# Optimization experiments

Hardware: AMD Instinct MI355X
Metric: run time of the kernel (lower is better)

The kernel has to match this reference:

```python
import jax, jax.numpy as jnp
import numpy as np

TEMP = 0.1
THR = 0.01
W_F = 8
HW0_I = (640, 640)
HW0_F = (320, 320)
HW1_F = (320, 320)
HW0_C = (80, 80)
HW1_C = (80, 80)


def setup_inputs() -> dict:
    key = jax.random.key(0)
    ks = jax.random.split(key, 12)
    M, WW, C, N = 8192, W_F * W_F, 96, 2
    Hf, Wf = HW0_F
    Hc, Wc = HW0_C
    inp = {}
    inp['feat_f0_unfold'] = jax.random.normal(ks[0], (M, WW, C), jnp.float32)
    inp['feat_f1_unfold'] = jax.random.normal(ks[1], (M, WW, C), jnp.float32)
    inp['feat_f0_whole'] = jax.random.normal(ks[2], (N, C, Hf, Wf), jnp.float32)
    inp['feat_f1_whole'] = jax.random.normal(ks[3], (N, C, Hf, Wf), jnp.float32)
    inp['b_ids_c'] = jax.random.randint(ks[4], (M,), 0, N, jnp.int32)
    # interior coarse cells so 3x3 subpixel gathers never go out of bounds
    r0 = jax.random.randint(ks[5], (M,), 1, Hc - 1, jnp.int32)
    c0 = jax.random.randint(ks[6], (M,), 1, Wc - 1, jnp.int32)
    r1 = jax.random.randint(ks[7], (M,), 1, Hc - 1, jnp.int32)
    c1 = jax.random.randint(ks[8], (M,), 1, Wc - 1, jnp.int32)
    inp['i_ids_c'] = r0 * Wc + c0
    inp['j_ids_c'] = r1 * Wc + c1
    dim2 = 2 * 96
    inp['w1'] = jax.random.normal(ks[9], (dim2, dim2, 3, 3), jnp.float32) * 0.02
    inp['w2'] = jax.random.normal(ks[10], (dim2, dim2, 3, 3), jnp.float32) * 0.02
    inp['w3'] = jax.random.normal(ks[11], (4, dim2, 1, 1), jnp.float32) * 0.02
    return inp


def _conv(x, w, stride, pad):
    return jax.lax.conv_general_dilated(
        x, w, window_strides=(stride, stride), padding=pad,
        dimension_numbers=('NCHW', 'OIHW', 'NCHW'))


def _gather_patch(whole, b, y, x):
    # whole: [N, C, H, W]; returns 3x3 patches centered at (y, x) with zero pad,
    # matching F.unfold(kernel_size=3, stride=1, padding=1) + index_select.
    pad = jnp.pad(whole, ((0, 0), (0, 0), (1, 1), (1, 1)))
    off = jnp.arange(3, dtype=y.dtype)
    rows = y[:, None] + off  # padded row indices y-1..y+1 -> y..y+2
    cols = x[:, None] + off
    p = pad[b[:, None, None], :, rows[:, :, None], cols[:, None, :]]  # [M,3,3,C]
    return p.transpose(0, 3, 1, 2)  # [M, C, 3, 3]


def reference(feat_f0_unfold, feat_f1_unfold, feat_f0_whole, feat_f1_whole,
              b_ids_c, i_ids_c, j_ids_c, w1, w2, w3):
    M, WW, C = feat_f0_unfold.shape
    inv = C ** -0.5
    sim = jnp.einsum('mlc,msc->mls', feat_f0_unfold * inv, feat_f1_unfold * inv) / TEMP
    conf = jax.nn.softmax(sim, axis=1) * jax.nn.softmax(sim, axis=2)  # [M, WW, WW]

    # top-1 per fine conf matrix (threshold AND global argmax per matrix)
    flat = conf.reshape(M, WW * WW)
    idx = jnp.argmax(flat, axis=1)
    mconf = jnp.max(flat, axis=1)
    valid = mconf > THR
    i_ids = idx // WW
    j_ids = idx % WW

    scale_f_c = HW0_F[0] // HW0_C[0]
    mk0c = jnp.stack([i_ids_c % HW0_C[1], i_ids_c // HW0_C[1]], axis=1) * scale_f_c
    mk1c = jnp.stack([j_ids_c % HW1_C[1], j_ids_c // HW1_C[1]], axis=1) * scale_f_c
    win0 = jnp.stack([i_ids % W_F, i_ids // W_F], axis=1)
    win1 = jnp.stack([j_ids % W_F, j_ids // W_F], axis=1)
    mk0_uns = mk0c + win0 - W_F // 2  # [M, 2] (x, y) fine-res int coords
    mk1_uns = mk1c + win1 - W_F // 2

    f0 = _gather_patch(feat_f0_whole, b_ids_c, mk0_uns[:, 1], mk0_uns[:, 0])
    f1 = _gather_patch(feat_f1_whole, b_ids_c, mk1_uns[:, 1], mk1_uns[:, 0])
    x = jnp.concatenate([f0, f1], axis=1)  # [M, 192*2? -> 192] actually 2*96=192
    x = jax.nn.leaky_relu(_conv(x, w1, 1, [(1, 1), (1, 1)]))
    x = jax.nn.leaky_relu(_conv(x, w2, 3, 'VALID'))
    x = _conv(x, w3, 1, 'VALID').reshape(M, 4)
    sub0 = jnp.tanh(x[:, :2]) * 0.5
    sub1 = jnp.tanh(x[:, 2:]) * 0.5

    scale = HW0_I[0] / HW0_F[0]
    mkpts0_f = (mk0_uns.astype(sub0.dtype) + sub0) * scale
    mkpts1_f = (mk1_uns.astype(sub1.dtype) + sub1) * scale
    mconf = jnp.where(valid, mconf, 0.0)
    return conf, mconf, mkpts0_f, mkpts1_f, valid
```

## Files before the change

kernel.cpp:

```cpp
#include <hip/hip_runtime.h>
#include <hip/hip_bf16.h>
#include <math.h>

typedef __attribute__((ext_vector_type(4))) float f32x4;
typedef __attribute__((ext_vector_type(8))) short bf16x8;

#define M_TOT   8192
#define OFF_MCONF 33554432LL
#define OFF_MK0   33562624LL
#define OFF_MK1   33579008LL
#define OFF_VALID 33595392LL
#define SIM_SCALE 0.10416666666666667f

__device__ __forceinline__ short f2bf(float v) {
    __hip_bfloat16 h = __float2bfloat16(v);
    return *reinterpret_cast<short*>(&h);
}

__global__ void wprep(const float* __restrict__ w1, const float* __restrict__ w2,
                      short* __restrict__ o1, short* __restrict__ o2) {
    int i = blockIdx.x * 256 + threadIdx.x;
    if (i >= 2 * 331776) return;
    const float* src = (i < 331776) ? w1 : w2;
    short* dst       = (i < 331776) ? o1 : o2;
    int o = (i < 331776) ? i : i - 331776;
    int oc = o / 1728, r = o % 1728;
    int q = r / 192, ic = r % 192;
    dst[o] = f2bf(src[oc * 1728 + ic * 9 + q]);
}

__global__ __launch_bounds__(256) void stageA(const float* __restrict__ f0u,
                                              const float* __restrict__ f1u,
                                              const int* __restrict__ i_ids_c,
                                              const int* __restrict__ j_ids_c,
                                              float* __restrict__ out,
                                              int* __restrict__ mkws) {
    __shared__ float f0L[64 * 100];
    __shared__ float f1L[64 * 100];
    __shared__ float Rpart[16 * 64];
    __shared__ float Cpart[16 * 64];
    __shared__ float invR[64], invC[64];
    __shared__ float rv[256];
    __shared__ int   ri[256];

    const int m = blockIdx.x;
    const int t = threadIdx.x;
    const int lg = t >> 4, sg = t & 15;

    const float* g0 = f0u + (size_t)m * 6144;
    const float* g1 = f1u + (size_t)m * 6144;
    for (int v = t; v < 1536; v += 256) {
        int l = v / 24, c4 = (v % 24) * 4;
        *(f32x4*)&f0L[l * 100 + c4] = *(const f32x4*)(g0 + v * 4);
        *(f32x4*)&f1L[l * 100 + c4] = *(const f32x4*)(g1 + v * 4);
    }
    __syncthreads();

    float acc[4][4] = {};
#pragma unroll 2
    for (int k = 0; k < 96; k += 4) {
        f32x4 a[4], b[4];
#pragma unroll
        for (int i = 0; i < 4; ++i) a[i] = *(const f32x4*)&f0L[(lg + 16 * i) * 100 + k];
#pragma unroll
        for (int j = 0; j < 4; ++j) b[j] = *(const f32x4*)&f1L[(sg + 16 * j) * 100 + k];
#pragma unroll
        for (int i = 0; i < 4; ++i)
#pragma unroll
            for (int j = 0; j < 4; ++j) {
                acc[i][j] += a[i].x * b[j].x;
                acc[i][j] += a[i].y * b[j].y;
                acc[i][j] += a[i].z * b[j].z;
                acc[i][j] += a[i].w * b[j].w;
            }
    }

    float e[4][4];
    float rp[4] = {0.f, 0.f, 0.f, 0.f}, cp[4] = {0.f, 0.f, 0.f, 0.f};
#pragma unroll
    for (int i = 0; i < 4; ++i)
#pragma unroll
        for (int j = 0; j < 4; ++j) {
            float v = __expf(acc[i][j] * SIM_SCALE);
            e[i][j] = v;
            rp[i] += v;
            cp[j] += v;
        }
#pragma unroll
    for (int i = 0; i < 4; ++i) Rpart[sg * 64 + lg + 16 * i] = rp[i];
#pragma unroll
    for (int j = 0; j < 4; ++j) Cpart[lg * 64 + sg + 16 * j] = cp[j];
    __syncthreads();
    if (t < 64) {
        float sR = 0.f, sC = 0.f;
#pragma unroll
        for (int g = 0; g < 16; ++g) { sR += Rpart[g * 64 + t]; sC += Cpart[g * 64 + t]; }
        invR[t] = 1.0f / sR;
        invC[t] = 1.0f / sC;
    }
    __syncthreads();

    float bestv = -1.0f;
    int besti = 0;
    float* cbase = out + (size_t)m * 4096;
#pragma unroll
    for (int i = 0; i < 4; ++i) {
        int l = lg + 16 * i;
        float iR = invR[l];
#pragma unroll
        for (int j = 0; j < 4; ++j) {
            int s = sg + 16 * j;
            float c = (e[i][j] * iR) * (e[i][j] * invC[s]);
            cbase[l * 64 + s] = c;
            int fi = l * 64 + s;
            if (c > bestv || (c == bestv && fi < besti)) { bestv = c; besti = fi; }
        }
    }
    rv[t] = bestv; ri[t] = besti;
    __syncthreads();
    if (t < 64) {
#pragma unroll
        for (int g = 1; g < 4; ++g) {
            float v = rv[t + 64 * g]; int idx = ri[t + 64 * g];
            if (v > rv[t] || (v == rv[t] && idx < ri[t])) { rv[t] = v; ri[t] = idx; }
        }
    }
    __syncthreads();
    if (t == 0) {
        float bv = rv[0]; int bi = ri[0];
        for (int g = 1; g < 64; ++g) {
            float v = rv[g]; int idx = ri[g];
            if (v > bv || (v == bv && idx < bi)) { bv = v; bi = idx; }
        }
        bool valid = bv > 0.01f;
        out[OFF_MCONF + m] = valid ? bv : 0.0f;
        out[OFF_VALID + m] = valid ? 1.0f : 0.0f;
        int il = bi >> 6, js = bi & 63;
        int ic0 = i_ids_c[m], jc0 = j_ids_c[m];
        mkws[m * 4 + 0] = (ic0 % 80) * 4 + (il & 7) - 4;
        mkws[m * 4 + 1] = (ic0 / 80) * 4 + (il >> 3) - 4;
        mkws[m * 4 + 2] = (jc0 % 80) * 4 + (js & 7) - 4;
        mkws[m * 4 + 3] = (jc0 / 80) * 4 + (js >> 3) - 4;
    }
}

__global__ __launch_bounds__(256, 2) void stageB(const float* __restrict__ w0whole,
                                                 const float* __restrict__ w1whole,
                                                 const int* __restrict__ bids,
                                                 const int* __restrict__ mkws,
                                                 const short* __restrict__ w1b,
                                                 const short* __restrict__ w2b,
                                                 const float* __restrict__ w3,
                                                 float* __restrict__ out) {
    __shared__ short bufA[32000];
    __shared__ float bufC[16 * 196];
    __shared__ float xout[64];

    const int t = threadIdx.x;
    const int m0 = blockIdx.x * 16;
    const int lane = t & 63, wv = t >> 6;
    const int l16 = lane & 15, quad = lane >> 4;
    const int colb = wv * 48;

    for (int v = t; v < 16 * 200; v += 256) {
        int mm = v / 200, c = v % 200;
        bufA[mm * 2000 + 1800 + c] = 0;
    }
    for (int seg = t; seg < 9216; seg += 256) {
        int c = seg % 96;
        int r = seg / 96;
        int dy = r % 3;
        int mi = r / 3;
        int img = mi & 1;
        int m_loc = mi >> 1;
        int mg = m0 + m_loc;
        int b = bids[mg];
        int mkx = mkws[mg * 4 + img * 2 + 0];
        int mky = mkws[mg * 4 + img * 2 + 1];
        int y = mky + dy - 1;
        const float* src = (img ? w1whole : w0whole) + (((size_t)b * 96 + c) * 320 + y) * 320;
        bool yok = (unsigned)y < 320u;
        short* dst = &bufA[m_loc * 2000 + dy * 3 * 200 + img * 96 + c];
#pragma unroll
        for (int dx = 0; dx < 3; ++dx) {
            int x = mkx + dx - 1;
            float v = (yok && (unsigned)x < 320u) ? src[x] : 0.0f;
            dst[dx * 200] = f2bf(v);
        }
    }
    __syncthreads();

    int mbase[9], py[9], px[9];
#pragma unroll
    for (int rt = 0; rt < 9; ++rt) {
        int row = rt * 16 + l16;
        int mm = row / 9;
        int p = row - mm * 9;
        mbase[rt] = mm * 2000;
        py[rt] = p / 3;
        px[rt] = p - py[rt] * 3;
    }
    f32x4 acc1[9][3] = {};
#pragma unroll
    for (int q = 0; q < 9; ++q) {
        const int qy = q / 3, qx = q % 3;
        int aoff[9];
#pragma unroll
        for (int rt = 0; rt < 9; ++rt) {
            int y = py[rt] + qy - 1, x = px[rt] + qx - 1;
            bool ok = ((unsigned)y < 3u) && ((unsigned)x < 3u);
            int slot = ok ? (y * 3 + x) : 9;
            aoff[rt] = mbase[rt] + slot * 200 + quad * 8;
        }
#pragma unroll
        for (int kk = 0; kk < 6; ++kk) {
            const int kg = q * 192 + kk * 32 + quad * 8;
            bf16x8 bfr[3];
#pragma unroll
            for (int ct = 0; ct < 3; ++ct) {
                int n = colb + ct * 16 + l16;
                bfr[ct] = *(const bf16x8*)(w1b + n * 1728 + kg);
            }
            bf16x8 afr[9];
#pragma unroll
            for (int rt = 0; rt < 9; ++rt)
                afr[rt] = *(const bf16x8*)&bufA[aoff[rt] + kk * 32];
#pragma unroll
            for (int rt = 0; rt < 9; ++rt)
#pragma unroll
                for (int ct = 0; ct < 3; ++ct)
                    acc1[rt][ct] = __builtin_amdgcn_mfma_f32_16x16x32_bf16(
                        afr[rt], bfr[ct], acc1[rt][ct], 0, 0, 0);
        }
    }
    __syncthreads();
#pragma unroll
    for (int rt = 0; rt < 9; ++rt)
#pragma unroll
        for (int ct = 0; ct < 3; ++ct)
#pragma unroll
            for (int r = 0; r < 4; ++r) {
                int row = rt * 16 + quad * 4 + r;
                int col = colb + ct * 16 + l16;
                float v = acc1[rt][ct][r];
                v = (v > 0.f) ? v : 0.01f * v;
                bufA[row * 200 + col] = f2bf(v);
            }
    __syncthreads();

    f32x4 acc2[3] = {};
#pragma unroll 6
    for (int ks = 0; ks < 54; ++ks) {
        int k = ks * 32 + quad * 8;
        int p = k / 192;
        int ic = k - p * 192;
        bf16x8 a = *(const bf16x8*)&bufA[l16 * 1800 + p * 200 + ic];
#pragma unroll
        for (int ct = 0; ct < 3; ++ct) {
            int n = colb + ct * 16 + l16;
            bf16x8 b = *(const bf16x8*)(w2b + n * 1728 + k);
            acc2[ct] = __builtin_amdgcn_mfma_f32_16x16x32_bf16(a, b, acc2[ct], 0, 0, 0);
        }
    }
#pragma unroll
    for (int ct = 0; ct < 3; ++ct)
#pragma unroll
        for (int r = 0; r < 4; ++r) {
            int mrow = quad * 4 + r;
            int col = colb + ct * 16 + l16;
            float v = acc2[ct][r];
            v = (v > 0.f) ? v : 0.01f * v;
            bufC[mrow * 196 + col] = v;
        }
    __syncthreads();

    if (t < 64) {
        int mloc = t >> 2, j = t & 3;
        const float* wr = w3 + j * 192;
        const float* xr = &bufC[mloc * 196];
        float d = 0.f;
        for (int c = 0; c < 192; ++c) d += xr[c] * wr[c];
        xout[t] = d;
    }
    __syncthreads();
    if (t < 16) {
        int mg = m0 + t;
        float s0x = tanhf(xout[t * 4 + 0]) * 0.5f;
        float s0y = tanhf(xout[t * 4 + 1]) * 0.5f;
        float s1x = tanhf(xout[t * 4 + 2]) * 0.5f;
        float s1y = tanhf(xout[t * 4 + 3]) * 0.5f;
        float mk0x = (float)mkws[mg * 4 + 0], mk0y = (float)mkws[mg * 4 + 1];
        float mk1x = (float)mkws[mg * 4 + 2], mk1y = (float)mkws[mg * 4 + 3];
        out[OFF_MK0 + mg * 2 + 0] = (mk0x + s0x) * 2.0f;
        out[OFF_MK0 + mg * 2 + 1] = (mk0y + s0y) * 2.0f;
        out[OFF_MK1 + mg * 2 + 0] = (mk1x + s1x) * 2.0f;
        out[OFF_MK1 + mg * 2 + 1] = (mk1y + s1y) * 2.0f;
    }
}

extern "C" void kernel_launch(void* const* d_in, const int* in_sizes, int n_in,
                              void* d_out, int out_size, void* d_ws, size_t ws_size,
                              hipStream_t stream) {
    const float* f0u = (const float*)d_in[0];
    const float* f1u = (const float*)d_in[1];
    const float* f0w = (const float*)d_in[2];
    const float* f1w = (const float*)d_in[3];
    const int* bids  = (const int*)d_in[4];
    const int* iids  = (const int*)d_in[5];
    const int* jids  = (const int*)d_in[6];
    const float* w1  = (const float*)d_in[7];
    const float* w2  = (const float*)d_in[8];
    const float* w3  = (const float*)d_in[9];
    float* out = (float*)d_out;
    char* ws = (char*)d_ws;
    int* mkws  = (int*)ws;
    short* w1b = (short*)(ws + 131072);
    short* w2b = (short*)(ws + 131072 + 663552);

    wprep<<<dim3(2592), dim3(256), 0, stream>>>(w1, w2, w1b, w2b);
    stageA<<<dim3(8192), dim3(256), 0, stream>>>(f0u, f1u, iids, jids, out, mkws);
    stageB<<<dim3(512), dim3(256), 0, stream>>>(f0w, f1w, bids, mkws, w1b, w2b, w3, out);
}
```

Baseline: 808.6 us.

## Compute similarity with split-bf16 MFMA and wave-shuffle softmax reductions in stageA

Replaces the scalar FP32 FMA similarity GEMM in stageA with bf16 MFMA 16x16x32 instructions. Each input is split into high and low bf16 parts, and three MFMAs per tile approximate FP32 accuracy. Row, column and argmax reductions now use wave shuffles instead of shared-memory arrays, which cuts LDS traffic and barriers, and launch bounds are raised to 3 blocks per CU. The cost is extra conversion work at load time and small precision differences compared with pure FP32.

```diff
diff --git a/kernel.cpp b/kernel.cpp
--- a/kernel.cpp
+++ b/kernel.cpp
@@ -4,6 +4,7 @@
 
 typedef __attribute__((ext_vector_type(4))) float f32x4;
 typedef __attribute__((ext_vector_type(8))) short bf16x8;
+typedef __attribute__((ext_vector_type(4))) short s16x4;
 
 #define M_TOT   8192
 #define OFF_MCONF 33554432LL
@@ -29,107 +30,130 @@
     dst[o] = f2bf(src[oc * 1728 + ic * 9 + q]);
 }
 
-__global__ __launch_bounds__(256) void stageA(const float* __restrict__ f0u,
-                                              const float* __restrict__ f1u,
-                                              const int* __restrict__ i_ids_c,
-                                              const int* __restrict__ j_ids_c,
-                                              float* __restrict__ out,
-                                              int* __restrict__ mkws) {
-    __shared__ float f0L[64 * 100];
-    __shared__ float f1L[64 * 100];
-    __shared__ float Rpart[16 * 64];
-    __shared__ float Cpart[16 * 64];
-    __shared__ float invR[64], invC[64];
-    __shared__ float rv[256];
-    __shared__ int   ri[256];
+__global__ __launch_bounds__(256, 3) void stageA(const float* __restrict__ f0u,
+                                                 const float* __restrict__ f1u,
+                                                 const int* __restrict__ i_ids_c,
+                                                 const int* __restrict__ j_ids_c,
+                                                 float* __restrict__ out,
+                                                 int* __restrict__ mkws) {
+    __shared__ short h0s[6144], l0s[6144];
+    __shared__ short h1s[6144], l1s[6144];
+    __shared__ float Cpart[256];
+    __shared__ float rbv[4];
+    __shared__ int   rbi[4];
 
     const int m = blockIdx.x;
     const int t = threadIdx.x;
-    const int lg = t >> 4, sg = t & 15;
+    const int lane = t & 63, w = t >> 6;
+    const int l15 = lane & 15, q = lane >> 4;
 
     const float* g0 = f0u + (size_t)m * 6144;
     const float* g1 = f1u + (size_t)m * 6144;
-    for (int v = t; v < 1536; v += 256) {
-        int l = v / 24, c4 = (v % 24) * 4;
-        *(f32x4*)&f0L[l * 100 + c4] = *(const f32x4*)(g0 + v * 4);
-        *(f32x4*)&f1L[l * 100 + c4] = *(const f32x4*)(g1 + v * 4);
-    }
-    __syncthreads();
-
-    float acc[4][4] = {};
-#pragma unroll 2
-    for (int k = 0; k < 96; k += 4) {
-        f32x4 a[4], b[4];
-#pragma unroll
-        for (int i = 0; i < 4; ++i) a[i] = *(const f32x4*)&f0L[(lg + 16 * i) * 100 + k];
-#pragma unroll
-        for (int j = 0; j < 4; ++j) b[j] = *(const f32x4*)&f1L[(sg + 16 * j) * 100 + k];
-#pragma unroll
-        for (int i = 0; i < 4; ++i)
-#pragma unroll
-            for (int j = 0; j < 4; ++j) {
-                acc[i][j] += a[i].x * b[j].x;
-                acc[i][j] += a[i].y * b[j].y;
-                acc[i][j] += a[i].z * b[j].z;
-                acc[i][j] += a[i].w * b[j].w;
-            }
+#pragma unroll
+    for (int it = 0; it < 12; ++it) {
+        const int i = it * 256 + t;
+        const bool first = (i < 1536);
+        const int off = (first ? i : i - 1536) * 4;
+        f32x4 v = *(const f32x4*)((first ? g0 : g1) + off);
+        s16x4 hv, lv;
+#pragma unroll
+        for (int j = 0; j < 4; ++j) {
+            __hip_bfloat16 hb = __float2bfloat16(v[j]);
+            hv[j] = *reinterpret_cast<short*>(&hb);
+            float r = v[j] - __bfloat162float(hb);
+            __hip_bfloat16 lb = __float2bfloat16(r);
+            lv[j] = *reinterpret_cast<short*>(&lb);
+        }
+        *(s16x4*)&(first ? h0s : h1s)[off] = hv;
+        *(s16x4*)&(first ? l0s : l1s)[off] = lv;
+    }
+    __syncthreads();
+
+    bf16x8 aH[3], aL[3];
+    const int abase = (w * 16 + l15) * 96;
+#pragma unroll
+    for (int c = 0; c < 3; ++c) {
+        aH[c] = *(const bf16x8*)&h0s[abase + c * 32 + q * 8];
+        aL[c] = *(const bf16x8*)&l0s[abase + c * 32 + q * 8];
+    }
+    f32x4 acc[4] = {};
+#pragma unroll
+    for (int sj = 0; sj < 4; ++sj) {
+        const int bbase = (sj * 16 + l15) * 96;
+#pragma unroll
+        for (int c = 0; c < 3; ++c) {
+            bf16x8 bH = *(const bf16x8*)&h1s[bbase + c * 32 + q * 8];
+            bf16x8 bL = *(const bf16x8*)&l1s[bbase + c * 32 + q * 8];
+            acc[sj] = __builtin_amdgcn_mfma_f32_16x16x32_bf16(aH[c], bH, acc[sj], 0, 0, 0);
+            acc[sj] = __builtin_amdgcn_mfma_f32_16x16x32_bf16(aH[c], bL, acc[sj], 0, 0, 0);
+            acc[sj] = __builtin_amdgcn_mfma_f32_16x16x32_bf16(aL[c], bH, acc[sj], 0, 0, 0);
+        }
     }
 
     float e[4][4];
     float rp[4] = {0.f, 0.f, 0.f, 0.f}, cp[4] = {0.f, 0.f, 0.f, 0.f};
 #pragma unroll
-    for (int i = 0; i < 4; ++i)
-#pragma unroll
-        for (int j = 0; j < 4; ++j) {
-            float v = __expf(acc[i][j] * SIM_SCALE);
-            e[i][j] = v;
-            rp[i] += v;
-            cp[j] += v;
-        }
-#pragma unroll
-    for (int i = 0; i < 4; ++i) Rpart[sg * 64 + lg + 16 * i] = rp[i];
-#pragma unroll
-    for (int j = 0; j < 4; ++j) Cpart[lg * 64 + sg + 16 * j] = cp[j];
-    __syncthreads();
-    if (t < 64) {
-        float sR = 0.f, sC = 0.f;
-#pragma unroll
-        for (int g = 0; g < 16; ++g) { sR += Rpart[g * 64 + t]; sC += Cpart[g * 64 + t]; }
-        invR[t] = 1.0f / sR;
-        invC[t] = 1.0f / sC;
-    }
-    __syncthreads();
+    for (int sj = 0; sj < 4; ++sj)
+#pragma unroll
+        for (int r = 0; r < 4; ++r) {
+            float v = __expf(acc[sj][r] * SIM_SCALE);
+            e[sj][r] = v;
+            rp[r] += v;
+            cp[sj] += v;
+        }
+#pragma unroll
+    for (int mk = 1; mk <= 8; mk <<= 1)
+#pragma unroll
+        for (int r = 0; r < 4; ++r) rp[r] += __shfl_xor(rp[r], mk);
+#pragma unroll
+    for (int mk = 16; mk <= 32; mk <<= 1)
+#pragma unroll
+        for (int sj = 0; sj < 4; ++sj) cp[sj] += __shfl_xor(cp[sj], mk);
+    if (q == 0) {
+#pragma unroll
+        for (int sj = 0; sj < 4; ++sj) Cpart[w * 64 + sj * 16 + l15] = cp[sj];
+    }
+    __syncthreads();
+
+    float ivr[4], ivc[4];
+#pragma unroll
+    for (int r = 0; r < 4; ++r) ivr[r] = 1.0f / rp[r];
+#pragma unroll
+    for (int sj = 0; sj < 4; ++sj) {
+        const int s = sj * 16 + l15;
+        ivc[sj] = 1.0f / (Cpart[s] + Cpart[64 + s] + Cpart[128 + s] + Cpart[192 + s]);
+    }
 
     float bestv = -1.0f;
     int besti = 0;
     float* cbase = out + (size_t)m * 4096;
 #pragma unroll
-    for (int i = 0; i < 4; ++i) {
-        int l = lg + 16 * i;
-        float iR = invR[l];
-#pragma unroll
-        for (int j = 0; j < 4; ++j) {
-            int s = sg + 16 * j;
-            float c = (e[i][j] * iR) * (e[i][j] * invC[s]);
-            cbase[l * 64 + s] = c;
-            int fi = l * 64 + s;
+    for (int sj = 0; sj < 4; ++sj) {
+        const int s = sj * 16 + l15;
+        const float is = ivc[sj];
+#pragma unroll
+        for (int r = 0; r < 4; ++r) {
+            const int row = w * 16 + q * 4 + r;
+            const float ev = e[sj][r];
+            const float c = (ev * ivr[r]) * (ev * is);
+            cbase[row * 64 + s] = c;
+            const int fi = row * 64 + s;
             if (c > bestv || (c == bestv && fi < besti)) { bestv = c; besti = fi; }
         }
     }
-    rv[t] = bestv; ri[t] = besti;
-    __syncthreads();
-    if (t < 64) {
+#pragma unroll
+    for (int mk = 1; mk <= 32; mk <<= 1) {
+        float ov = __shfl_xor(bestv, mk);
+        int   oi = __shfl_xor(besti, mk);
+        if (ov > bestv || (ov == bestv && oi < besti)) { bestv = ov; besti = oi; }
+    }
+    if (lane == 0) { rbv[w] = bestv; rbi[w] = besti; }
+    __syncthreads();
+    if (t == 0) {
+        float bv = rbv[0]; int bi = rbi[0];
 #pragma unroll
         for (int g = 1; g < 4; ++g) {
-            float v = rv[t + 64 * g]; int idx = ri[t + 64 * g];
-            if (v > rv[t] || (v == rv[t] && idx < ri[t])) { rv[t] = v; ri[t] = idx; }
-        }
-    }
-    __syncthreads();
-    if (t == 0) {
-        float bv = rv[0]; int bi = ri[0];
-        for (int g = 1; g < 64; ++g) {
-            float v = rv[g]; int idx = ri[g];
+            float v = rbv[g]; int idx = rbi[g];
             if (v > bv || (v == bv && idx < bi)) { bv = v; bi = idx; }
         }
         bool valid = bv > 0.01f;
```

Result: faster. 690.4 us (-14.6%).
